# Kernel optimization log

Hardware: AMD Instinct MI355X
Metric: run time of the kernel (lower is better)

The kernel has to match this reference:

```python
import jax, jax.numpy as jnp
import numpy as np

B, S, D = 2, 2048, 1024
H = 16
HD = D // H  # 64
THETA = 10000.0


def apply_rope(x, positions, theta):
    # x: (b, h, s, hd); positions: (s,)
    hd = x.shape[-1]
    inv_freq = theta ** (-jnp.arange(0, hd, 2, dtype=jnp.float32) / hd)  # (hd/2,)
    angles = positions.astype(jnp.float32)[:, None] * inv_freq[None, :]  # (s, hd/2)
    cos, sin = jnp.cos(angles), jnp.sin(angles)
    x1 = x[..., 0::2]
    x2 = x[..., 1::2]
    r1 = x1 * cos - x2 * sin
    r2 = x1 * sin + x2 * cos
    out = jnp.stack([r1, r2], axis=-1).reshape(x.shape)
    return out.astype(x.dtype)


def setup_inputs() -> dict:
    key = jax.random.key(0)
    ks = jax.random.split(key, 5)
    scale = 1.0 / np.sqrt(D)
    return {
        "in_features": jax.random.normal(ks[0], (B, S, D), dtype=jnp.float32),
        "token_positions": jnp.arange(S, dtype=jnp.int32),
        "Wq": jax.random.normal(ks[1], (D, D), dtype=jnp.float32) * scale,
        "Wk": jax.random.normal(ks[2], (D, D), dtype=jnp.float32) * scale,
        "Wv": jax.random.normal(ks[3], (D, D), dtype=jnp.float32) * scale,
        "Wo": jax.random.normal(ks[4], (D, D), dtype=jnp.float32) * scale,
    }


def reference(in_features, token_positions, Wq, Wk, Wv, Wo):
    b, s, d = in_features.shape
    h, hd = H, HD
    # bias-free linear: y = x @ W.T  (W is (out, in))
    q = in_features @ Wq.T
    k = in_features @ Wk.T
    v = in_features @ Wv.T
    # (b, s, h*hd) -> (b, h, s, hd)
    split = lambda t: t.reshape(b, s, h, hd).transpose(0, 2, 1, 3)
    q, k, v = split(q), split(k), split(v)
    q = apply_rope(q, token_positions, THETA)
    k = apply_rope(k, token_positions, THETA)
    scores = jnp.einsum("bhid,bhjd->bhij", q, k) / jnp.sqrt(jnp.asarray(hd, dtype=q.dtype))
    causal = jnp.triu(jnp.ones((s, s), dtype=bool), k=1)
    scores = jnp.where(causal, -jnp.inf, scores)
    attn = jax.nn.softmax(scores, axis=-1)
    out = jnp.einsum("bhij,bhjd->bhid", attn, v)
    out = out.transpose(0, 2, 1, 3).reshape(b, s, d)
    return out @ Wo.T
```

## Files before the change

kernel.cpp:

```cpp
#include <hip/hip_runtime.h>
#include <math.h>

#define NUM_HEADS 16
#define HEAD_DIM 64

typedef __bf16 bf16x8 __attribute__((ext_vector_type(8)));
typedef short shortx4 __attribute__((ext_vector_type(4)));
typedef float floatx4 __attribute__((ext_vector_type(4)));

#if __has_builtin(__builtin_amdgcn_exp2f)
#define EXP2(x) __builtin_amdgcn_exp2f(x)
#else
#define EXP2(x) exp2f(x)
#endif

__device__ __forceinline__ unsigned short f2b(float f) {
  unsigned int u = __float_as_uint(f);
  u += 0x7fffu + ((u >> 16) & 1u);
  return (unsigned short)(u >> 16);
}

__device__ __forceinline__ void async16(const void* g, void* l) {
  __builtin_amdgcn_global_load_lds(
      (const __attribute__((address_space(1))) unsigned int*)g,
      (__attribute__((address_space(3))) unsigned int*)l, 16, 0, 0);
}

__device__ __forceinline__ void cvt4(const float* in, unsigned short* out, int i) {
  float4 v = ((const float4*)in)[i];
  ushort4 o;
  o.x = f2b(v.x); o.y = f2b(v.y); o.z = f2b(v.z); o.w = f2b(v.w);
  ((ushort4*)out)[i] = o;
}

__global__ void prep(const float* __restrict__ x,
                     const float* __restrict__ w0, const float* __restrict__ w1,
                     const float* __restrict__ w2, const float* __restrict__ w3,
                     const int* __restrict__ pos,
                     unsigned short* Xb, unsigned short* o0, unsigned short* o1,
                     unsigned short* o2, unsigned short* o3,
                     float* __restrict__ tab, int xq, int w4, int ntab) {
  int i = blockIdx.x * 256 + threadIdx.x;
  int z = blockIdx.y;
  if (z == 0) {
    if (i < xq) {
#pragma unroll
      for (int rep = 0; rep < 4; ++rep) cvt4(x, Xb, rep * xq + i);
    }
  } else if (z <= 4) {
    if (i < w4) {
      const float* in = (z == 1) ? w0 : (z == 2) ? w1 : (z == 3) ? w2 : w3;
      unsigned short* out = (z == 1) ? o0 : (z == 2) ? o1 : (z == 3) ? o2 : o3;
      cvt4(in, out, i);
    }
  } else {
    if (i < ntab) {
      int fi = i & 31, s = i >> 5;
      float inv = expf(-0.28782313662425575f * (float)fi);
      float ang = (float)pos[s] * inv;
      float sn, cs;
      sincosf(ang, &sn, &cs);
      tab[i * 2] = cs;
      tab[i * 2 + 1] = sn;
    }
  }
}

template <int MODE, int MT>
__global__ __launch_bounds__(256, MODE == 1 ? 4 : 2)
void gemm_bt(const unsigned short* __restrict__ A,
             const unsigned short* __restrict__ B0,
             const unsigned short* __restrict__ B1,
             const unsigned short* __restrict__ B2,
             void* out0v, void* out1v, void* out2v,
             const float* __restrict__ ctab,
             int M, int N, int K, int S) {
  __shared__ unsigned short As[(MT / 16) * 512];
  __shared__ unsigned short Bs[8 * 512];
  const int tid = threadIdx.x;
  const int lane = tid & 63;
  const int w = tid >> 6;
  const int lane16 = lane & 15;
  const int g = lane >> 4;
  const int wm = w >> 1, wn = w & 1;
  const int m0 = blockIdx.y * MT;
  const int n0 = blockIdx.x * 128;
  const unsigned short* Bp = (blockIdx.z == 0) ? B0 : (blockIdx.z == 1 ? B1 : B2);
  constexpr int MTILES = MT / 32;

  const floatx4 vzero = {0.f, 0.f, 0.f, 0.f};
  floatx4 acc[MTILES][4];
#pragma unroll
  for (int i = 0; i < MTILES; i++)
#pragma unroll
    for (int j = 0; j < 4; j++) acc[i][j] = vzero;

  const int ar = lane >> 2;
  const int ac = (lane & 3) * 8;

  for (int k0 = 0; k0 < K; k0 += 32) {
    if constexpr (MT == 128) {
#pragma unroll
      for (int c = 0; c < 2; c++) {
        int chunk = w * 2 + c;
        async16(A  + (size_t)(m0 + chunk * 16 + ar) * K + k0 + ac, As + chunk * 512);
        async16(Bp + (size_t)(n0 + chunk * 16 + ar) * K + k0 + ac, Bs + chunk * 512);
      }
    } else {
      async16(A  + (size_t)(m0 + w * 16 + ar) * K + k0 + ac, As + w * 512);
      async16(Bp + (size_t)(n0 + w * 16 + ar) * K + k0 + ac, Bs + w * 512);
      async16(Bp + (size_t)(n0 + (w + 4) * 16 + ar) * K + k0 + ac, Bs + (w + 4) * 512);
    }
    __syncthreads();
    bf16x8 a[MTILES], b[4];
#pragma unroll
    for (int mt = 0; mt < MTILES; mt++)
      a[mt] = *(const bf16x8*)&As[(wm * (MT / 2) + mt * 16 + lane16) * 32 + g * 8];
#pragma unroll
    for (int nt = 0; nt < 4; nt++)
      b[nt] = *(const bf16x8*)&Bs[(wn * 64 + nt * 16 + lane16) * 32 + g * 8];
#pragma unroll
    for (int mt = 0; mt < MTILES; mt++)
#pragma unroll
      for (int nt = 0; nt < 4; nt++)
        acc[mt][nt] = __builtin_amdgcn_mfma_f32_16x16x32_bf16(b[nt], a[mt], acc[mt][nt], 0, 0, 0);
    __syncthreads();
  }

  if (MODE == 0) {
    if (blockIdx.z < 2) {
      unsigned short* outp = (unsigned short*)((blockIdx.z == 0) ? out0v : out1v);
      const float qs = (blockIdx.z == 0) ? 0.18033688011112042f : 1.0f;
#pragma unroll
      for (int mt = 0; mt < MTILES; mt++) {
        int m = m0 + wm * (MT / 2) + mt * 16 + lane16;
        int bb = m / S, s = m - bb * S;
        const float* crow = ctab + (size_t)s * 64;
#pragma unroll
        for (int nt = 0; nt < 4; nt++) {
          int n = n0 + wn * 64 + nt * 16 + g * 4;
          int h = n >> 6, dl = n & 63;
          floatx4 v = acc[mt][nt];
          float4 cs = *(const float4*)&crow[dl];
          float r0 = (v[0] * cs.x - v[1] * cs.y) * qs;
          float r1 = (v[0] * cs.y + v[1] * cs.x) * qs;
          float r2 = (v[2] * cs.z - v[3] * cs.w) * qs;
          float r3 = (v[2] * cs.w + v[3] * cs.z) * qs;
          shortx4 st;
          st[0] = (short)f2b(r0); st[1] = (short)f2b(r1);
          st[2] = (short)f2b(r2); st[3] = (short)f2b(r3);
          *(shortx4*)&outp[(((size_t)(bb * NUM_HEADS + h) * S + s) << 6) + dl] = st;
        }
      }
    } else {
      unsigned short* outp = (unsigned short*)out2v;
#pragma unroll
      for (int mt = 0; mt < MTILES; mt++) {
        int m = m0 + wm * (MT / 2) + mt * 16 + lane16;
        int bb = m / S, s = m - bb * S;
#pragma unroll
        for (int nt = 0; nt < 4; nt++) {
          int n = n0 + wn * 64 + nt * 16 + g * 4;
          int bh = bb * NUM_HEADS + (n >> 6);
          int dl = n & 63;
          size_t dbase = ((size_t)bh * 64 + dl) * S + s;
#pragma unroll
          for (int r = 0; r < 4; r++)
            outp[dbase + (size_t)r * S] = f2b(acc[mt][nt][r]);
        }
      }
    }
  } else {
    float* outp = (float*)out0v;
#pragma unroll
    for (int mt = 0; mt < MTILES; mt++) {
      int m = m0 + wm * (MT / 2) + mt * 16 + lane16;
#pragma unroll
      for (int nt = 0; nt < 4; nt++) {
        int n = n0 + wn * 64 + nt * 16 + g * 4;
        *(floatx4*)&outp[(size_t)m * N + n] = acc[mt][nt];
      }
    }
  }
}

__global__ __launch_bounds__(256, 2)
void flash_attn7(const unsigned short* __restrict__ Q,
                 const unsigned short* __restrict__ Kv,
                 const unsigned short* __restrict__ Vt,
                 unsigned short* __restrict__ Oattn, int S) {
  __shared__ unsigned short Ks[4 * 4096];
  __shared__ unsigned short Vs[4 * 4096];
  const int tid = threadIdx.x;
  const int lane = tid & 63;
  const int w = tid >> 6;
  const int lane16 = lane & 15;
  const int g = lane >> 4;
  const int sw = lane16 & 7;
  const int NT = S >> 6;
  int qa, bh;
  {
    int nx = gridDim.x, ny = gridDim.y;
    int flat = blockIdx.y * nx + blockIdx.x;
    if ((ny & 7) == 0) {
      int xcd = flat & 7;
      int idx = flat >> 3;
      int per = ny >> 3;
      bh = xcd * per + (idx % per);
      qa = idx / per;
    } else {
      qa = blockIdx.x; bh = blockIdx.y;
    }
  }
  const int qb = NT - 1 - qa;
  const int b = bh >> 4, h = bh & 15;
  const size_t kbase = (size_t)bh * S * HEAD_DIM;
  const unsigned short* Kbase = Kv + kbase;
  const unsigned short* Vtbase = Vt + (size_t)bh * HEAD_DIM * S;
  const int qrowA = qa * 64 + w * 16;
  const int qrowB = qb * 64 + w * 16;

  bf16x8 qA0, qA1, qB0, qB1;
  {
    const unsigned short* qp = Q + kbase + (size_t)(qrowA + lane16) * HEAD_DIM + g * 8;
    qA0 = *(const bf16x8*)qp;
    qA1 = *(const bf16x8*)(qp + 32);
    qp = Q + kbase + (size_t)(qrowB + lane16) * HEAD_DIM + g * 8;
    qB0 = *(const bf16x8*)qp;
    qB1 = *(const bf16x8*)(qp + 32);
  }

  const int ci0 = w * 64 + lane;
  const int ci1 = ci0 + 256;
  const int r0 = ci0 >> 3, j0 = (ci0 & 7) ^ (r0 & 7);
  const int r1 = ci1 >> 3, j1 = (ci1 & 7) ^ (r1 & 7);
  const unsigned short* kS0 = Kbase + r0 * HEAD_DIM + j0 * 8;
  const unsigned short* kS1 = Kbase + r1 * HEAD_DIM + j1 * 8;
  const unsigned short* vS0 = Vtbase + (size_t)r0 * S + j0 * 8;
  const unsigned short* vS1 = Vtbase + (size_t)r1 * S + j1 * 8;
  unsigned short* kD0 = Ks + ci0 * 8;
  unsigned short* kD1 = Ks + ci1 * 8;
  unsigned short* vD0 = Vs + ci0 * 8;
  unsigned short* vD1 = Vs + ci1 * 8;

  auto stage = [&](int t, int bi) {
    int koff = t * 4096;
    int voff = t * 64;
    int doff = bi * 4096;
    async16(kS0 + koff, kD0 + doff);
    async16(kS1 + koff, kD1 + doff);
    async16(vS0 + voff, vD0 + doff);
    async16(vS1 + voff, vD1 + doff);
  };

  const floatx4 vzero = {0.f, 0.f, 0.f, 0.f};
  floatx4 oA[4], oB[4];
#pragma unroll
  for (int i = 0; i < 4; i++) { oA[i] = vzero; oB[i] = vzero; }
  float lA = 0.f, lB = 0.f;

  stage(0, 0);
  __builtin_amdgcn_sched_barrier(0);
  if (qb >= 1) stage(1, 1);
  __builtin_amdgcn_sched_barrier(0);
  if (qb >= 2) stage(2, 2);
  __builtin_amdgcn_sched_barrier(0);

  for (int t = 0; t <= qb; ++t) {
    const int bi = t & 3;
    const int rem = qb - t;
    if (rem >= 2)      asm volatile("s_waitcnt vmcnt(8)" ::: "memory");
    else if (rem == 1) asm volatile("s_waitcnt vmcnt(4)" ::: "memory");
    else               asm volatile("s_waitcnt vmcnt(0)" ::: "memory");
    __builtin_amdgcn_sched_barrier(0);
    __builtin_amdgcn_s_barrier();
    __builtin_amdgcn_sched_barrier(0);
    if (t + 3 <= qb) stage(t + 3, (t + 3) & 3);
    __builtin_amdgcn_sched_barrier(0);

    const unsigned short* Kb_ = Ks + bi * 4096;
    const unsigned short* Vb_ = Vs + bi * 4096;
    const bool doA = (t <= qa);

    bf16x8 kf0[4], kf1[4];
#pragma unroll
    for (int c = 0; c < 4; ++c) {
      int rr = c * 16 + lane16;
      kf0[c] = *(const bf16x8*)&Kb_[(rr * 8 + (g ^ sw)) * 8];
      kf1[c] = *(const bf16x8*)&Kb_[(rr * 8 + ((4 + g) ^ sw)) * 8];
    }

    floatx4 scB[4];
#pragma unroll
    for (int c = 0; c < 4; ++c) {
      floatx4 s = vzero;
      s = __builtin_amdgcn_mfma_f32_16x16x32_bf16(kf0[c], qB0, s, 0, 0, 0);
      s = __builtin_amdgcn_mfma_f32_16x16x32_bf16(kf1[c], qB1, s, 0, 0, 0);
      scB[c] = s;
    }
    if (t == qb) {
      const int i = qrowB + lane16;
      const int jb = t * 64;
#pragma unroll
      for (int c = 0; c < 4; ++c)
#pragma unroll
        for (int r = 0; r < 4; ++r)
          if (jb + c * 16 + g * 4 + r > i) scB[c][r] = -INFINITY;
    }
    shortx4 pcB[4], pcA[4];
#pragma unroll
    for (int c = 0; c < 4; ++c) {
      float p0 = EXP2(scB[c][0]);
      float p1 = EXP2(scB[c][1]);
      float p2 = EXP2(scB[c][2]);
      float p3 = EXP2(scB[c][3]);
      lB += (p0 + p1) + (p2 + p3);
      union { unsigned int u[2]; shortx4 s4; } pu;
      pu.u[0] = __builtin_amdgcn_perm(__float_as_uint(p1), __float_as_uint(p0), 0x07060302u);
      pu.u[1] = __builtin_amdgcn_perm(__float_as_uint(p3), __float_as_uint(p2), 0x07060302u);
      pcB[c] = pu.s4;
    }

    if (doA) {
      floatx4 scA[4];
#pragma unroll
      for (int c = 0; c < 4; ++c) {
        floatx4 s = vzero;
        s = __builtin_amdgcn_mfma_f32_16x16x32_bf16(kf0[c], qA0, s, 0, 0, 0);
        s = __builtin_amdgcn_mfma_f32_16x16x32_bf16(kf1[c], qA1, s, 0, 0, 0);
        scA[c] = s;
      }
      if (t == qa) {
        const int i = qrowA + lane16;
        const int jb = t * 64;
#pragma unroll
        for (int c = 0; c < 4; ++c)
#pragma unroll
          for (int r = 0; r < 4; ++r)
            if (jb + c * 16 + g * 4 + r > i) scA[c][r] = -INFINITY;
      }
#pragma unroll
      for (int c = 0; c < 4; ++c) {
        float p0 = EXP2(scA[c][0]);
        float p1 = EXP2(scA[c][1]);
        float p2 = EXP2(scA[c][2]);
        float p3 = EXP2(scA[c][3]);
        lA += (p0 + p1) + (p2 + p3);
        union { unsigned int u[2]; shortx4 s4; } pu;
        pu.u[0] = __builtin_amdgcn_perm(__float_as_uint(p1), __float_as_uint(p0), 0x07060302u);
        pu.u[1] = __builtin_amdgcn_perm(__float_as_uint(p3), __float_as_uint(p2), 0x07060302u);
        pcA[c] = pu.s4;
      }
#pragma unroll
      for (int nt = 0; nt < 4; ++nt) {
        int rv = nt * 16 + lane16;
#pragma unroll
        for (int c = 0; c < 4; ++c) {
          shortx4 vf = *(const shortx4*)&Vb_[(rv * 8 + ((c * 2 + (g >> 1)) ^ sw)) * 8 + (g & 1) * 4];
          oB[nt] = __builtin_amdgcn_mfma_f32_16x16x16bf16_1k(vf, pcB[c], oB[nt], 0, 0, 0);
          oA[nt] = __builtin_amdgcn_mfma_f32_16x16x16bf16_1k(vf, pcA[c], oA[nt], 0, 0, 0);
        }
      }
    } else {
#pragma unroll
      for (int nt = 0; nt < 4; ++nt) {
        int rv = nt * 16 + lane16;
#pragma unroll
        for (int c = 0; c < 4; ++c) {
          shortx4 vf = *(const shortx4*)&Vb_[(rv * 8 + ((c * 2 + (g >> 1)) ^ sw)) * 8 + (g & 1) * 4];
          oB[nt] = __builtin_amdgcn_mfma_f32_16x16x16bf16_1k(vf, pcB[c], oB[nt], 0, 0, 0);
        }
      }
    }
  }

  {
    float l = lA;
    l += __shfl_xor(l, 16, 64);
    l += __shfl_xor(l, 32, 64);
    float inv = 1.0f / l;
    int srow = qrowA + lane16;
    size_t rowb = ((size_t)b * S + srow) * 1024 + h * 64;
#pragma unroll
    for (int nt = 0; nt < 4; ++nt) {
      shortx4 st;
#pragma unroll
      for (int r = 0; r < 4; ++r) st[r] = (short)f2b(oA[nt][r] * inv);
      *(shortx4*)&Oattn[rowb + nt * 16 + g * 4] = st;
    }
  }
  {
    float l = lB;
    l += __shfl_xor(l, 16, 64);
    l += __shfl_xor(l, 32, 64);
    float inv = 1.0f / l;
    int srow = qrowB + lane16;
    size_t rowb = ((size_t)b * S + srow) * 1024 + h * 64;
#pragma unroll
    for (int nt = 0; nt < 4; ++nt) {
      shortx4 st;
#pragma unroll
      for (int r = 0; r < 4; ++r) st[r] = (short)f2b(oB[nt][r] * inv);
      *(shortx4*)&Oattn[rowb + nt * 16 + g * 4] = st;
    }
  }
}

extern "C" void kernel_launch(void* const* d_in, const int* in_sizes, int n_in,
                              void* d_out, int out_size, void* d_ws, size_t ws_size,
                              hipStream_t stream) {
  const float* x  = (const float*)d_in[0];
  const int*  pos = (const int*)d_in[1];
  const float* wq = (const float*)d_in[2];
  const float* wk = (const float*)d_in[3];
  const float* wv = (const float*)d_in[4];
  const float* wo = (const float*)d_in[5];

  const int D = 1024;
  const int S = in_sizes[1];
  const int M = in_sizes[0] / D;
  const int B = M / S;
  const int BH = B * NUM_HEADS;

  char* wsb = (char*)d_ws;
  size_t off = 0;
  auto alloc = [&](size_t bytes) {
    char* p = wsb + off;
    off += (bytes + 255) & ~(size_t)255;
    return p;
  };
  unsigned short* Xb   = (unsigned short*)alloc((size_t)M * D * 2);
  unsigned short* Wqb  = (unsigned short*)alloc((size_t)D * D * 2);
  unsigned short* Wkb  = (unsigned short*)alloc((size_t)D * D * 2);
  unsigned short* Wvb  = (unsigned short*)alloc((size_t)D * D * 2);
  unsigned short* Wob  = (unsigned short*)alloc((size_t)D * D * 2);
  unsigned short* Qb   = (unsigned short*)alloc((size_t)M * D * 2);
  unsigned short* Kb   = (unsigned short*)alloc((size_t)M * D * 2);
  unsigned short* Vtb  = (unsigned short*)alloc((size_t)M * D * 2);
  unsigned short* Attn = (unsigned short*)alloc((size_t)M * D * 2);
  float*          Ctab = (float*)alloc((size_t)S * 32 * 2 * 4);
  (void)ws_size;

  {
    int n4x = M * D / 4;
    int xq = n4x / 4;
    int w4 = D * D / 4;
    int ntab = S * 32;
    int gx = (w4 + 255) / 256;
    prep<<<dim3(gx, 6), 256, 0, stream>>>(x, wq, wk, wv, wo, pos,
                                          Xb, Wqb, Wkb, Wvb, Wob, Ctab,
                                          xq, w4, ntab);
  }
  gemm_bt<0, 128><<<dim3(D / 128, M / 128, 3), 256, 0, stream>>>(
      Xb, Wqb, Wkb, Wvb, Qb, Kb, Vtb, Ctab, M, D, D, S);
  flash_attn7<<<dim3(S / 128, BH), 256, 0, stream>>>(Qb, Kb, Vtb, Attn, S);
  gemm_bt<1, 64><<<dim3(D / 128, M / 64, 1), 256, 0, stream>>>(
      Attn, Wob, Wob, Wob, d_out, d_out, d_out, Ctab, M, D, D, S);
}
```

Baseline: 178.8 us.

## Share K/V tiles across two query-pair groups in 512-thread attention blocks

```diff
diff --git a/kernel.cpp b/kernel.cpp
--- a/kernel.cpp
+++ b/kernel.cpp
@@ -184,8 +184,8 @@
   }
 }
 
-__global__ __launch_bounds__(256, 2)
-void flash_attn7(const unsigned short* __restrict__ Q,
+__global__ __launch_bounds__(512, 2)
+void flash_attn8(const unsigned short* __restrict__ Q,
                  const unsigned short* __restrict__ Kv,
                  const unsigned short* __restrict__ Vt,
                  unsigned short* __restrict__ Oattn, int S) {
@@ -194,11 +194,13 @@
   const int tid = threadIdx.x;
   const int lane = tid & 63;
   const int w = tid >> 6;
+  const int g2 = w >> 2;
+  const int wq = w & 3;
   const int lane16 = lane & 15;
   const int g = lane >> 4;
   const int sw = lane16 & 7;
   const int NT = S >> 6;
-  int qa, bh;
+  int iblk, bh;
   {
     int nx = gridDim.x, ny = gridDim.y;
     int flat = blockIdx.y * nx + blockIdx.x;
@@ -207,18 +209,20 @@
       int idx = flat >> 3;
       int per = ny >> 3;
       bh = xcd * per + (idx % per);
-      qa = idx / per;
+      iblk = idx / per;
     } else {
-      qa = blockIdx.x; bh = blockIdx.y;
-    }
-  }
-  const int qb = NT - 1 - qa;
+      iblk = blockIdx.x; bh = blockIdx.y;
+    }
+  }
+  const int myqa = 2 * iblk + g2;
+  const int myqb = NT - 1 - 2 * iblk - g2;
+  const int tmax = NT - 1 - 2 * iblk;
   const int b = bh >> 4, h = bh & 15;
   const size_t kbase = (size_t)bh * S * HEAD_DIM;
   const unsigned short* Kbase = Kv + kbase;
   const unsigned short* Vtbase = Vt + (size_t)bh * HEAD_DIM * S;
-  const int qrowA = qa * 64 + w * 16;
-  const int qrowB = qb * 64 + w * 16;
+  const int qrowA = myqa * 64 + wq * 16;
+  const int qrowB = myqb * 64 + wq * 16;
 
   bf16x8 qA0, qA1, qB0, qB1;
   {
@@ -230,27 +234,17 @@
     qB1 = *(const bf16x8*)(qp + 32);
   }
 
-  const int ci0 = w * 64 + lane;
-  const int ci1 = ci0 + 256;
-  const int r0 = ci0 >> 3, j0 = (ci0 & 7) ^ (r0 & 7);
-  const int r1 = ci1 >> 3, j1 = (ci1 & 7) ^ (r1 & 7);
-  const unsigned short* kS0 = Kbase + r0 * HEAD_DIM + j0 * 8;
-  const unsigned short* kS1 = Kbase + r1 * HEAD_DIM + j1 * 8;
-  const unsigned short* vS0 = Vtbase + (size_t)r0 * S + j0 * 8;
-  const unsigned short* vS1 = Vtbase + (size_t)r1 * S + j1 * 8;
-  unsigned short* kD0 = Ks + ci0 * 8;
-  unsigned short* kD1 = Ks + ci1 * 8;
-  unsigned short* vD0 = Vs + ci0 * 8;
-  unsigned short* vD1 = Vs + ci1 * 8;
+  const int ci = tid;
+  const int r = ci >> 3, j = (ci & 7) ^ (r & 7);
+  const unsigned short* kS = Kbase + r * HEAD_DIM + j * 8;
+  const unsigned short* vS = Vtbase + (size_t)r * S + j * 8;
+  unsigned short* kD = Ks + ci * 8;
+  unsigned short* vD = Vs + ci * 8;
 
   auto stage = [&](int t, int bi) {
-    int koff = t * 4096;
-    int voff = t * 64;
     int doff = bi * 4096;
-    async16(kS0 + koff, kD0 + doff);
-    async16(kS1 + koff, kD1 + doff);
-    async16(vS0 + voff, vD0 + doff);
-    async16(vS1 + voff, vD1 + doff);
+    async16(kS + t * 4096, kD + doff);
+    async16(vS + t * 64, vD + doff);
   };
 
   const floatx4 vzero = {0.f, 0.f, 0.f, 0.f};
@@ -261,114 +255,117 @@
 
   stage(0, 0);
   __builtin_amdgcn_sched_barrier(0);
-  if (qb >= 1) stage(1, 1);
+  if (tmax >= 1) stage(1, 1);
   __builtin_amdgcn_sched_barrier(0);
-  if (qb >= 2) stage(2, 2);
+  if (tmax >= 2) stage(2, 2);
   __builtin_amdgcn_sched_barrier(0);
 
-  for (int t = 0; t <= qb; ++t) {
+  for (int t = 0; t <= tmax; ++t) {
     const int bi = t & 3;
-    const int rem = qb - t;
-    if (rem >= 2)      asm volatile("s_waitcnt vmcnt(8)" ::: "memory");
-    else if (rem == 1) asm volatile("s_waitcnt vmcnt(4)" ::: "memory");
+    const int rem = tmax - t;
+    if (rem >= 2)      asm volatile("s_waitcnt vmcnt(4)" ::: "memory");
+    else if (rem == 1) asm volatile("s_waitcnt vmcnt(2)" ::: "memory");
     else               asm volatile("s_waitcnt vmcnt(0)" ::: "memory");
     __builtin_amdgcn_sched_barrier(0);
     __builtin_amdgcn_s_barrier();
     __builtin_amdgcn_sched_barrier(0);
-    if (t + 3 <= qb) stage(t + 3, (t + 3) & 3);
+    if (t + 3 <= tmax) stage(t + 3, (t + 3) & 3);
     __builtin_amdgcn_sched_barrier(0);
 
-    const unsigned short* Kb_ = Ks + bi * 4096;
-    const unsigned short* Vb_ = Vs + bi * 4096;
-    const bool doA = (t <= qa);
-
-    bf16x8 kf0[4], kf1[4];
-#pragma unroll
-    for (int c = 0; c < 4; ++c) {
-      int rr = c * 16 + lane16;
-      kf0[c] = *(const bf16x8*)&Kb_[(rr * 8 + (g ^ sw)) * 8];
-      kf1[c] = *(const bf16x8*)&Kb_[(rr * 8 + ((4 + g) ^ sw)) * 8];
-    }
-
-    floatx4 scB[4];
-#pragma unroll
-    for (int c = 0; c < 4; ++c) {
-      floatx4 s = vzero;
-      s = __builtin_amdgcn_mfma_f32_16x16x32_bf16(kf0[c], qB0, s, 0, 0, 0);
-      s = __builtin_amdgcn_mfma_f32_16x16x32_bf16(kf1[c], qB1, s, 0, 0, 0);
-      scB[c] = s;
-    }
-    if (t == qb) {
-      const int i = qrowB + lane16;
-      const int jb = t * 64;
-#pragma unroll
-      for (int c = 0; c < 4; ++c)
-#pragma unroll
-        for (int r = 0; r < 4; ++r)
-          if (jb + c * 16 + g * 4 + r > i) scB[c][r] = -INFINITY;
-    }
-    shortx4 pcB[4], pcA[4];
-#pragma unroll
-    for (int c = 0; c < 4; ++c) {
-      float p0 = EXP2(scB[c][0]);
-      float p1 = EXP2(scB[c][1]);
-      float p2 = EXP2(scB[c][2]);
-      float p3 = EXP2(scB[c][3]);
-      lB += (p0 + p1) + (p2 + p3);
-      union { unsigned int u[2]; shortx4 s4; } pu;
-      pu.u[0] = __builtin_amdgcn_perm(__float_as_uint(p1), __float_as_uint(p0), 0x07060302u);
-      pu.u[1] = __builtin_amdgcn_perm(__float_as_uint(p3), __float_as_uint(p2), 0x07060302u);
-      pcB[c] = pu.s4;
-    }
-
-    if (doA) {
-      floatx4 scA[4];
+    const bool doB = (t <= myqb);
+    const bool doA = (t <= myqa);
+    if (doB) {
+      const unsigned short* Kb_ = Ks + bi * 4096;
+      const unsigned short* Vb_ = Vs + bi * 4096;
+
+      bf16x8 kf0[4], kf1[4];
+#pragma unroll
+      for (int c = 0; c < 4; ++c) {
+        int rr = c * 16 + lane16;
+        kf0[c] = *(const bf16x8*)&Kb_[(rr * 8 + (g ^ sw)) * 8];
+        kf1[c] = *(const bf16x8*)&Kb_[(rr * 8 + ((4 + g) ^ sw)) * 8];
+      }
+
+      floatx4 scB[4];
 #pragma unroll
       for (int c = 0; c < 4; ++c) {
         floatx4 s = vzero;
-        s = __builtin_amdgcn_mfma_f32_16x16x32_bf16(kf0[c], qA0, s, 0, 0, 0);
-        s = __builtin_amdgcn_mfma_f32_16x16x32_bf16(kf1[c], qA1, s, 0, 0, 0);
-        scA[c] = s;
-      }
-      if (t == qa) {
-        const int i = qrowA + lane16;
+        s = __builtin_amdgcn_mfma_f32_16x16x32_bf16(kf0[c], qB0, s, 0, 0, 0);
+        s = __builtin_amdgcn_mfma_f32_16x16x32_bf16(kf1[c], qB1, s, 0, 0, 0);
+        scB[c] = s;
+      }
+      if (t == myqb) {
+        const int i = qrowB + lane16;
         const int jb = t * 64;
 #pragma unroll
         for (int c = 0; c < 4; ++c)
 #pragma unroll
-          for (int r = 0; r < 4; ++r)
-            if (jb + c * 16 + g * 4 + r > i) scA[c][r] = -INFINITY;
-      }
+          for (int rr = 0; rr < 4; ++rr)
+            if (jb + c * 16 + g * 4 + rr > i) scB[c][rr] = -INFINITY;
+      }
+      shortx4 pcB[4], pcA[4];
 #pragma unroll
       for (int c = 0; c < 4; ++c) {
-        float p0 = EXP2(scA[c][0]);
-        float p1 = EXP2(scA[c][1]);
-        float p2 = EXP2(scA[c][2]);
-        float p3 = EXP2(scA[c][3]);
-        lA += (p0 + p1) + (p2 + p3);
+        float p0 = EXP2(scB[c][0]);
+        float p1 = EXP2(scB[c][1]);
+        float p2 = EXP2(scB[c][2]);
+        float p3 = EXP2(scB[c][3]);
+        lB += (p0 + p1) + (p2 + p3);
         union { unsigned int u[2]; shortx4 s4; } pu;
         pu.u[0] = __builtin_amdgcn_perm(__float_as_uint(p1), __float_as_uint(p0), 0x07060302u);
         pu.u[1] = __builtin_amdgcn_perm(__float_as_uint(p3), __float_as_uint(p2), 0x07060302u);
-        pcA[c] = pu.s4;
-      }
-#pragma unroll
-      for (int nt = 0; nt < 4; ++nt) {
-        int rv = nt * 16 + lane16;
+        pcB[c] = pu.s4;
+      }
+
+      if (doA) {
+        floatx4 scA[4];
 #pragma unroll
         for (int c = 0; c < 4; ++c) {
-          shortx4 vf = *(const shortx4*)&Vb_[(rv * 8 + ((c * 2 + (g >> 1)) ^ sw)) * 8 + (g & 1) * 4];
-          oB[nt] = __builtin_amdgcn_mfma_f32_16x16x16bf16_1k(vf, pcB[c], oB[nt], 0, 0, 0);
-          oA[nt] = __builtin_amdgcn_mfma_f32_16x16x16bf16_1k(vf, pcA[c], oA[nt], 0, 0, 0);
-        }
-      }
-    } else {
-#pragma unroll
-      for (int nt = 0; nt < 4; ++nt) {
-        int rv = nt * 16 + lane16;
+          floatx4 s = vzero;
+          s = __builtin_amdgcn_mfma_f32_16x16x32_bf16(kf0[c], qA0, s, 0, 0, 0);
+          s = __builtin_amdgcn_mfma_f32_16x16x32_bf16(kf1[c], qA1, s, 0, 0, 0);
+          scA[c] = s;
+        }
+        if (t == myqa) {
+          const int i = qrowA + lane16;
+          const int jb = t * 64;
+#pragma unroll
+          for (int c = 0; c < 4; ++c)
+#pragma unroll
+            for (int rr = 0; rr < 4; ++rr)
+              if (jb + c * 16 + g * 4 + rr > i) scA[c][rr] = -INFINITY;
+        }
 #pragma unroll
         for (int c = 0; c < 4; ++c) {
-          shortx4 vf = *(const shortx4*)&Vb_[(rv * 8 + ((c * 2 + (g >> 1)) ^ sw)) * 8 + (g & 1) * 4];
-          oB[nt] = __builtin_amdgcn_mfma_f32_16x16x16bf16_1k(vf, pcB[c], oB[nt], 0, 0, 0);
+          float p0 = EXP2(scA[c][0]);
+          float p1 = EXP2(scA[c][1]);
+          float p2 = EXP2(scA[c][2]);
+          float p3 = EXP2(scA[c][3]);
+          lA += (p0 + p1) + (p2 + p3);
+          union { unsigned int u[2]; shortx4 s4; } pu;
+          pu.u[0] = __builtin_amdgcn_perm(__float_as_uint(p1), __float_as_uint(p0), 0x07060302u);
+          pu.u[1] = __builtin_amdgcn_perm(__float_as_uint(p3), __float_as_uint(p2), 0x07060302u);
+          pcA[c] = pu.s4;
+        }
+#pragma unroll
+        for (int nt = 0; nt < 4; ++nt) {
+          int rv = nt * 16 + lane16;
+#pragma unroll
+          for (int c = 0; c < 4; ++c) {
+            shortx4 vf = *(const shortx4*)&Vb_[(rv * 8 + ((c * 2 + (g >> 1)) ^ sw)) * 8 + (g & 1) * 4];
+            oB[nt] = __builtin_amdgcn_mfma_f32_16x16x16bf16_1k(vf, pcB[c], oB[nt], 0, 0, 0);
+            oA[nt] = __builtin_amdgcn_mfma_f32_16x16x16bf16_1k(vf, pcA[c], oA[nt], 0, 0, 0);
+          }
+        }
+      } else {
+#pragma unroll
+        for (int nt = 0; nt < 4; ++nt) {
+          int rv = nt * 16 + lane16;
+#pragma unroll
+          for (int c = 0; c < 4; ++c) {
+            shortx4 vf = *(const shortx4*)&Vb_[(rv * 8 + ((c * 2 + (g >> 1)) ^ sw)) * 8 + (g & 1) * 4];
+            oB[nt] = __builtin_amdgcn_mfma_f32_16x16x16bf16_1k(vf, pcB[c], oB[nt], 0, 0, 0);
+          }
         }
       }
     }
@@ -385,7 +382,7 @@
     for (int nt = 0; nt < 4; ++nt) {
       shortx4 st;
 #pragma unroll
-      for (int r = 0; r < 4; ++r) st[r] = (short)f2b(oA[nt][r] * inv);
+      for (int rr = 0; rr < 4; ++rr) st[rr] = (short)f2b(oA[nt][rr] * inv);
       *(shortx4*)&Oattn[rowb + nt * 16 + g * 4] = st;
     }
   }
@@ -400,7 +397,7 @@
     for (int nt = 0; nt < 4; ++nt) {
       shortx4 st;
 #pragma unroll
-      for (int r = 0; r < 4; ++r) st[r] = (short)f2b(oB[nt][r] * inv);
+      for (int rr = 0; rr < 4; ++rr) st[rr] = (short)f2b(oB[nt][rr] * inv);
       *(shortx4*)&Oattn[rowb + nt * 16 + g * 4] = st;
     }
   }
@@ -453,7 +450,7 @@
   }
   gemm_bt<0, 128><<<dim3(D / 128, M / 128, 3), 256, 0, stream>>>(
       Xb, Wqb, Wkb, Wvb, Qb, Kb, Vtb, Ctab, M, D, D, S);
-  flash_attn7<<<dim3(S / 128, BH), 256, 0, stream>>>(Qb, Kb, Vtb, Attn, S);
+  flash_attn8<<<dim3(S / 256, BH), 512, 0, stream>>>(Qb, Kb, Vtb, Attn, S);
   gemm_bt<1, 64><<<dim3(D / 128, M / 64, 1), 256, 0, stream>>>(
       Attn, Wob, Wob, Wob, d_out, d_out, d_out, Ctab, M, D, D, S);
 }
```

After: 183.1 us. 2.4% more time.

## Triple-buffer GEMM shared-memory tiles with async prefetch two stages ahead

Applied to the files above, without the earlier changes.

```diff
diff --git a/kernel.cpp b/kernel.cpp
--- a/kernel.cpp
+++ b/kernel.cpp
@@ -75,8 +75,10 @@
              void* out0v, void* out1v, void* out2v,
              const float* __restrict__ ctab,
              int M, int N, int K, int S) {
-  __shared__ unsigned short As[(MT / 16) * 512];
-  __shared__ unsigned short Bs[8 * 512];
+  constexpr int ABUF = (MT / 16) * 512;
+  constexpr int BBUF = 8 * 512;
+  __shared__ unsigned short As[3 * ABUF];
+  __shared__ unsigned short Bs[3 * BBUF];
   const int tid = threadIdx.x;
   const int lane = tid & 63;
   const int w = tid >> 6;
@@ -98,33 +100,58 @@
   const int ar = lane >> 2;
   const int ac = (lane & 3) * 8;
 
-  for (int k0 = 0; k0 < K; k0 += 32) {
+  auto stageg = [&](int k0, int sbi) {
     if constexpr (MT == 128) {
 #pragma unroll
       for (int c = 0; c < 2; c++) {
         int chunk = w * 2 + c;
-        async16(A  + (size_t)(m0 + chunk * 16 + ar) * K + k0 + ac, As + chunk * 512);
-        async16(Bp + (size_t)(n0 + chunk * 16 + ar) * K + k0 + ac, Bs + chunk * 512);
+        async16(A  + (size_t)(m0 + chunk * 16 + ar) * K + k0 + ac, As + sbi * ABUF + chunk * 512);
+        async16(Bp + (size_t)(n0 + chunk * 16 + ar) * K + k0 + ac, Bs + sbi * BBUF + chunk * 512);
       }
     } else {
-      async16(A  + (size_t)(m0 + w * 16 + ar) * K + k0 + ac, As + w * 512);
-      async16(Bp + (size_t)(n0 + w * 16 + ar) * K + k0 + ac, Bs + w * 512);
-      async16(Bp + (size_t)(n0 + (w + 4) * 16 + ar) * K + k0 + ac, Bs + (w + 4) * 512);
-    }
-    __syncthreads();
+      async16(A  + (size_t)(m0 + w * 16 + ar) * K + k0 + ac, As + sbi * ABUF + w * 512);
+      async16(Bp + (size_t)(n0 + w * 16 + ar) * K + k0 + ac, Bs + sbi * BBUF + w * 512);
+      async16(Bp + (size_t)(n0 + (w + 4) * 16 + ar) * K + k0 + ac, Bs + sbi * BBUF + (w + 4) * 512);
+    }
+  };
+
+  const int NK = K >> 5;
+  stageg(0, 0);
+  __builtin_amdgcn_sched_barrier(0);
+  if (NK > 1) stageg(32, 1);
+  __builtin_amdgcn_sched_barrier(0);
+
+  int bi = 0, si = 2;
+  for (int ks = 0; ks < NK; ++ks) {
+    if (ks < NK - 1) {
+      if constexpr (MT == 128) asm volatile("s_waitcnt vmcnt(4)" ::: "memory");
+      else                     asm volatile("s_waitcnt vmcnt(3)" ::: "memory");
+    } else {
+      asm volatile("s_waitcnt vmcnt(0)" ::: "memory");
+    }
+    __builtin_amdgcn_sched_barrier(0);
+    __builtin_amdgcn_s_barrier();
+    __builtin_amdgcn_sched_barrier(0);
+    if (ks + 2 < NK) stageg((ks + 2) << 5, si);
+    __builtin_amdgcn_sched_barrier(0);
+
+    const unsigned short* Ab = As + bi * ABUF;
+    const unsigned short* Bb = Bs + bi * BBUF;
     bf16x8 a[MTILES], b[4];
 #pragma unroll
     for (int mt = 0; mt < MTILES; mt++)
-      a[mt] = *(const bf16x8*)&As[(wm * (MT / 2) + mt * 16 + lane16) * 32 + g * 8];
+      a[mt] = *(const bf16x8*)&Ab[(wm * (MT / 2) + mt * 16 + lane16) * 32 + g * 8];
 #pragma unroll
     for (int nt = 0; nt < 4; nt++)
-      b[nt] = *(const bf16x8*)&Bs[(wn * 64 + nt * 16 + lane16) * 32 + g * 8];
+      b[nt] = *(const bf16x8*)&Bb[(wn * 64 + nt * 16 + lane16) * 32 + g * 8];
 #pragma unroll
     for (int mt = 0; mt < MTILES; mt++)
 #pragma unroll
       for (int nt = 0; nt < 4; nt++)
         acc[mt][nt] = __builtin_amdgcn_mfma_f32_16x16x32_bf16(b[nt], a[mt], acc[mt][nt], 0, 0, 0);
-    __syncthreads();
+
+    bi = (bi == 2) ? 0 : bi + 1;
+    si = (si == 2) ? 0 : si + 1;
   }
 
   if (MODE == 0) {
```

After: 180.4 us. Within noise of the previous version (+0.9%).
